# Performance work log

Measured on AMD Instinct MI355X. Metric: run time of the kernel, lower is better.

## Reference

```python
import jax, jax.numpy as jnp
import numpy as np

BATCH, SEQ, D = 128, 256, 64


def setup_inputs() -> dict:
    key = jax.random.key(0)
    k1, k2, k3 = jax.random.split(key, 3)
    eye = jnp.eye(D, dtype=jnp.float32)
    return {
        "x": jax.random.normal(k1, (BATCH, D), dtype=jnp.float32),
        "U_t": jax.random.normal(k2, (BATCH, SEQ, D), dtype=jnp.float32),
        "Y_t": jax.random.normal(k3, (BATCH, SEQ, D), dtype=jnp.float32),
        # learnable params, 'identity' init per module
        "F_mat": eye,
        "B_mat": eye,
        "H": eye,
        "LQ": jnp.tril(eye),
        "LR": jnp.tril(eye),
    }


def _kalman(x, U_t, Y_t, F_mat, B_mat, H, LQ, LR):
    d = x.shape[-1]
    bsz = x.shape[0]
    Q = LQ @ LQ.T                      # [D,D] process noise cov
    R = LR @ LR.T                      # [D,D] measurement noise cov
    I = jnp.eye(d, dtype=x.dtype)
    P0 = jnp.broadcast_to(I, (bsz, d, d))

    def step(carry, inp):
        x_prev, P = carry              # [B,D], [B,D,D]
        u, y = inp                     # [B,D], [B,D,D]
        x_pred = x_prev @ F_mat.T + u @ B_mat.T
        P_pred = F_mat @ P @ F_mat.T + Q            # broadcasts [D,D]@[B,D,D]
        S = H @ P_pred @ H.T + R                    # [B,D,D]
        S_inv = jnp.linalg.inv(S)
        K = P_pred @ (H.T @ S_inv)                  # Kalman gain [B,D,D]
        innov = y - x_pred @ H.T                    # [B,D]
        # matches torch: (innov.unsqueeze(1) @ K).squeeze(1)
        x_new = x_pred + jnp.einsum('bd,bde->be', innov, K)
        IKH = I - K @ H
        P_new = IKH @ P_pred @ jnp.swapaxes(IKH, -1, -2) \
              + K @ R @ jnp.swapaxes(K, -1, -2)
        P_new = 0.5 * (P_new + jnp.swapaxes(P_new, -1, -2))  # symmetrize
        return (x_new, P_new), (x_new, P_new)

    inputs = (jnp.swapaxes(U_t, 0, 1), jnp.swapaxes(Y_t, 0, 1))  # [S,B,D]
    _, (preds, covs) = jax.lax.scan(step, (x, P0), inputs)
    # prediction [B,S,D], covariance [B,S,D,D]
    return jnp.swapaxes(preds, 0, 1), jnp.swapaxes(covs, 0, 1)


def reference(x, U_t, Y_t, F_mat, B_mat, H, LQ, LR):
    return _kalman(x, U_t, Y_t, F_mat, B_mat, H, LQ, LR)
```

## Files before the change

kernel.cpp:

```cpp
#include <hip/hip_runtime.h>

#define BATCH 128
#define SEQ   256

#define WS_K  16
#define WS_A  (16 + SEQ * 4096)
#define WS_BP (WS_A + 4096)
#define WS_KS (WS_BP + 4096)

typedef unsigned short u16;
typedef float  f32x4v __attribute__((ext_vector_type(4)));
typedef __bf16 bf16x8 __attribute__((ext_vector_type(8)));
typedef unsigned short u16x8 __attribute__((ext_vector_type(8)));

struct Acc { f32x4v t[2][2]; };

__device__ __forceinline__ u16 bf16hi(float x) {
  unsigned u = __float_as_uint(x);
  return (u16)((u + 0x7fffu + ((u >> 16) & 1u)) >> 16);
}
__device__ __forceinline__ float bf16f(u16 h) {
  return __uint_as_float(((unsigned)h) << 16);
}

__device__ __forceinline__ int swadr(int a, int c) {
  return a * 64 + ((c ^ (a & 7)) << 3);
}

__device__ __forceinline__ bf16x8 frag(const u16* M, int strip, int kb, int q, int ln) {
  return *(const bf16x8*)(M + swadr(strip * 16 + ln, kb * 4 + q));
}

__device__ __forceinline__ void mm(const u16* As, const u16* Bs, Acc& acc,
                                   int R, int Cb, int q, int ln) {
#pragma unroll
  for (int kb = 0; kb < 2; ++kb) {
    bf16x8 ah[2], al[2], bh[2], bl[2];
#pragma unroll
    for (int i = 0; i < 2; ++i) {
      ah[i] = frag(As,        2 * R  + i, kb, q, ln);
      al[i] = frag(As + 4096, 2 * R  + i, kb, q, ln);
      bh[i] = frag(Bs,        2 * Cb + i, kb, q, ln);
      bl[i] = frag(Bs + 4096, 2 * Cb + i, kb, q, ln);
    }
#pragma unroll
    for (int i = 0; i < 2; ++i)
#pragma unroll
      for (int j = 0; j < 2; ++j) {
        acc.t[i][j] = __builtin_amdgcn_mfma_f32_16x16x32_bf16(ah[i], bh[j], acc.t[i][j], 0, 0, 0);
        acc.t[i][j] = __builtin_amdgcn_mfma_f32_16x16x32_bf16(ah[i], bl[j], acc.t[i][j], 0, 0, 0);
        acc.t[i][j] = __builtin_amdgcn_mfma_f32_16x16x32_bf16(al[i], bh[j], acc.t[i][j], 0, 0, 0);
      }
  }
}

__device__ __forceinline__ Acc accZero() {
  Acc a;
#pragma unroll
  for (int i = 0; i < 2; ++i)
#pragma unroll
    for (int j = 0; j < 2; ++j) {
      f32x4v z; z.x = 0.f; z.y = 0.f; z.z = 0.f; z.w = 0.f;
      a.t[i][j] = z;
    }
  return a;
}

__device__ __forceinline__ void storeC(float* dst, const Acc& a, int R, int Cb, int q, int ln) {
#pragma unroll
  for (int i = 0; i < 2; ++i)
#pragma unroll
    for (int j = 0; j < 2; ++j)
#pragma unroll
      for (int k = 0; k < 4; ++k)
        dst[(32 * R + 16 * i + 4 * q + k) * 64 + 32 * Cb + 16 * j + ln] = a.t[i][j][k];
}

__device__ __forceinline__ void emit16(const float* v, int row, int cb, u16* Rs, u16* Ts) {
  u16 h[16], lo[16];
#pragma unroll
  for (int e = 0; e < 16; ++e) {
    h[e] = bf16hi(v[e]);
    lo[e] = bf16hi(v[e] - bf16f(h[e]));
  }
  if (Rs) {
#pragma unroll
    for (int c = 0; c < 2; ++c) {
      u16x8 vh, vl;
#pragma unroll
      for (int e = 0; e < 8; ++e) { vh[e] = h[8 * c + e]; vl[e] = lo[8 * c + e]; }
      const int ad = swadr(row, (cb >> 3) + c);
      *(u16x8*)(Rs + ad) = vh;
      *(u16x8*)(Rs + 4096 + ad) = vl;
    }
  }
  if (Ts) {
    const int rc = row >> 3, rr = row & 7;
#pragma unroll
    for (int e = 0; e < 16; ++e) {
      const int a = cb + e;
      const int ad = a * 64 + ((rc ^ (a & 7)) << 3) + rr;
      Ts[ad] = h[e];
      Ts[4096 + ad] = lo[e];
    }
  }
}

__device__ __forceinline__ void splitsrc(const float* src, u16* Rs, u16* Ts,
                                         int mode, float scale, float dval, int tid) {
  const int row = tid >> 2, cb = (tid & 3) << 4;
  float v[16];
#pragma unroll
  for (int m = 0; m < 4; ++m) {
    f32x4v x = *(const f32x4v*)(src + row * 64 + cb + 4 * m);
    v[4 * m] = x.x; v[4 * m + 1] = x.y; v[4 * m + 2] = x.z; v[4 * m + 3] = x.w;
  }
  if (mode == 1) {
#pragma unroll
    for (int e = 0; e < 16; ++e) v[e] *= scale;
  } else if (mode == 2) {
#pragma unroll
    for (int e = 0; e < 16; ++e) v[e] = (((cb + e) == row) ? dval : 0.f) - v[e];
  }
  emit16(v, row, cb, Rs, Ts);
}

__device__ __forceinline__ float redmax(float v, float* red, int tid) {
#pragma unroll
  for (int off = 32; off > 0; off >>= 1) v = fmaxf(v, __shfl_xor(v, off));
  if ((tid & 63) == 0) red[300 + (tid >> 6)] = v;
  __syncthreads();
  float m = fmaxf(fmaxf(red[300], red[301]), fmaxf(red[302], red[303]));
  __syncthreads();
  return m;
}

__device__ __forceinline__ float dot4(float4 a, float4 b, float acc) {
  return fmaf(a.x, b.x, fmaf(a.y, b.y, fmaf(a.z, b.z, fmaf(a.w, b.w, acc))));
}

__global__ void __launch_bounds__(256, 1)
k1_riccati(const float* __restrict__ Fg, const float* __restrict__ Bg,
           const float* __restrict__ Hg, const float* __restrict__ LQg,
           const float* __restrict__ LRg, float* __restrict__ ws,
           float* __restrict__ covs) {
  __shared__ __align__(16) u16 smb[7 * 8192];
  __shared__ __align__(16) float Mf32[4096];
  __shared__ __align__(16) float Ppf32[4096];
  __shared__ __align__(16) float red[308];

  const int tid = threadIdx.x;
  const int l = tid & 63, w = tid >> 6, q = l >> 4, ln = l & 15;
  const int R = w >> 1, Cb = w & 1;

  {
    const int row = tid >> 2, cb = (tid & 3) << 4;
    float od = 0.f;
    const float* mats[5] = {Fg, Bg, Hg, LQg, LRg};
#pragma unroll
    for (int mi = 0; mi < 5; ++mi) {
      const float* M = mats[mi];
#pragma unroll
      for (int m = 0; m < 4; ++m) {
        f32x4v x = *(const f32x4v*)(M + row * 64 + cb + 4 * m);
        const int j0c = cb + 4 * m;
        if (j0c + 0 != row) od = fmaxf(od, fabsf(x.x));
        if (j0c + 1 != row) od = fmaxf(od, fabsf(x.y));
        if (j0c + 2 != row) od = fmaxf(od, fabsf(x.z));
        if (j0c + 3 != row) od = fmaxf(od, fabsf(x.w));
      }
    }
    const float odall = redmax(od, red, tid);
    if (odall == 0.f) {
      if (tid < 64) {
        const int e = tid;
        const float f = Fg[e * 65], b = Bg[e * 65], h = Hg[e * 65];
        const float lq = LQg[e * 65], lr = LRg[e * 65];
        const float qv = lq * lq, rv = lr * lr;
        float p = 1.f, kprev = 0.f, kcur = 0.f, om = 1.f;
        int tstar = SEQ - 1;
        for (int t = 0; t < SEQ; ++t) {
          const float pp = f * p * f + qv;
          const float s = h * pp * h + rv;
          const float k = pp * h / s;
          const float kh = k * h;
          const float omv = 1.f - kh;
          const float pn = omv * omv * pp + k * k * rv;
          float* Kt = ws + WS_K + (size_t)t * 4096 + e * 64;
          float* Ct = covs + (size_t)t * 4096 + e * 64;
          f32x4v z; z.x = 0.f; z.y = 0.f; z.z = 0.f; z.w = 0.f;
#pragma unroll
          for (int m = 0; m < 16; ++m) {
            *(f32x4v*)(Kt + 4 * m) = z;
            *(f32x4v*)(Ct + 4 * m) = z;
          }
          Kt[e] = k;
          Ct[e] = pn;
          float dk = (t == 0) ? 1e9f : fabsf(k - kprev);
#pragma unroll
          for (int off = 32; off > 0; off >>= 1) dk = fmaxf(dk, __shfl_xor(dk, off));
          p = pn; kprev = k; kcur = k; om = omv;
          if (dk < 1e-3f) { tstar = t; break; }
        }
        {
          const float astar = om * f, bpv = om * b;
          float* Ar = ws + WS_A + e * 64;
          float* Bp = ws + WS_BP + e * 64;
          float* Ks = ws + WS_KS + e * 64;
          f32x4v z; z.x = 0.f; z.y = 0.f; z.z = 0.f; z.w = 0.f;
#pragma unroll
          for (int m = 0; m < 16; ++m) {
            *(f32x4v*)(Ar + 4 * m) = z;
            *(f32x4v*)(Bp + 4 * m) = z;
            *(f32x4v*)(Ks + 4 * m) = z;
          }
          Ar[e] = astar; Bp[e] = bpv; Ks[e] = kcur;
          const float a2 = astar * astar, a4 = a2 * a2, a8 = a4 * a4;
          float a16 = fabsf(a8 * a8);
#pragma unroll
          for (int off = 32; off > 0; off >>= 1) a16 = fmaxf(a16, __shfl_xor(a16, off));
          if (e == 0) {
            ((int*)ws)[0] = tstar;
            ((int*)ws)[1] = (tstar <= 16 && a16 < 1e-5f) ? 1 : 0;
          }
        }
      }
      return;
    }
  }

  u16* SF = smb;
  u16* SH = smb + 8192;
  u16* SX = smb + 2 * 8192;
  u16* S1 = smb + 3 * 8192;
  u16* S2 = smb + 4 * 8192;
  u16* S3 = smb + 5 * 8192;
  u16* S4 = smb + 6 * 8192;

  splitsrc(Fg, SF, nullptr, 0, 0, 0, tid);
  splitsrc(Hg, SH, nullptr, 0, 0, 0, tid);
  splitsrc(LQg, S1, nullptr, 0, 0, 0, tid);
  __syncthreads();
  Acc qacc = accZero(); mm(S1, S1, qacc, R, Cb, q, ln);
  __syncthreads();
  splitsrc(LRg, S1, nullptr, 0, 0, 0, tid);
  __syncthreads();
  Acc racc = accZero(); mm(S1, S1, racc, R, Cb, q, ln);
  __syncthreads();
  {
    const int row = tid >> 2, cb = (tid & 3) << 4;
    float v[16];
#pragma unroll
    for (int e = 0; e < 16; ++e) v[e] = ((cb + e) == row) ? 1.f : 0.f;
    emit16(v, row, cb, S4, nullptr);
  }
  __syncthreads();

  int tstar = SEQ - 1;
  for (int t = 0; t < SEQ; ++t) {
    const u16* Wsrc = SF;
    if (t > 0) {
      Acc a = accZero(); mm(SF, S4, a, R, Cb, q, ln);
      storeC(Mf32, a, R, Cb, q, ln);
      __syncthreads();
      splitsrc(Mf32, S1, nullptr, 0, 0, 0, tid);
      __syncthreads();
      Wsrc = S1;
    }
    {
      Acc a = qacc; mm(Wsrc, SF, a, R, Cb, q, ln);
      storeC(Ppf32, a, R, Cb, q, ln);
      __syncthreads();
      splitsrc(Ppf32, S2, nullptr, 0, 0, 0, tid);
      __syncthreads();
    }
    {
      Acc a = accZero(); mm(SH, S2, a, R, Cb, q, ln);
      storeC(Mf32, a, R, Cb, q, ln);
      __syncthreads();
      splitsrc(Mf32, S3, S4, 0, 0, 0, tid);
      __syncthreads();
    }
    {
      Acc a = racc; mm(S3, SH, a, R, Cb, q, ln);
      storeC(Mf32, a, R, Cb, q, ln);
      __syncthreads();
      if (t == 0) {
        const int col = tid & 63, grp = tid >> 6;
        float s = 0.f;
        for (int r2 = grp * 16; r2 < grp * 16 + 16; ++r2) s += fabsf(Mf32[r2 * 64 + col]);
        red[tid] = s;
        __syncthreads();
        if (tid < 64) {
          float cs = red[tid] + red[64 + tid] + red[128 + tid] + red[192 + tid];
#pragma unroll
          for (int off = 32; off > 0; off >>= 1) cs = fmaxf(cs, __shfl_xor(cs, off));
          if (tid == 0) red[256] = 1.f / (cs * cs);
        }
        __syncthreads();
        const float sc = red[256];
        splitsrc(Mf32, SX, nullptr, 1, sc, 0, tid);
        __syncthreads();
      }
      splitsrc(Mf32, S2, nullptr, 0, 0, 0, tid);
      __syncthreads();
    }
    const int cap = (t == 0) ? 40 : 4;
    for (int it = 0; it < cap; ++it) {
      Acc e_ = accZero(); mm(S2, SX, e_, R, Cb, q, ln);
      float r = 0.f;
#pragma unroll
      for (int i = 0; i < 2; ++i)
#pragma unroll
        for (int j = 0; j < 2; ++j)
#pragma unroll
          for (int k = 0; k < 4; ++k) {
            const int gr = 32 * R + 16 * i + 4 * q + k;
            const int gc = 32 * Cb + 16 * j + ln;
            r = fmaxf(r, fabsf(e_.t[i][j][k] - ((gr == gc) ? 1.f : 0.f)));
          }
      const float rall = redmax(r, red, tid);
      if (rall < 5e-4f) break;
      storeC(Mf32, e_, R, Cb, q, ln);
      __syncthreads();
      splitsrc(Mf32, nullptr, S1, 2, 0, 2.0f, tid);
      __syncthreads();
      Acc x2 = accZero(); mm(SX, S1, x2, R, Cb, q, ln);
      storeC(Mf32, x2, R, Cb, q, ln);
      __syncthreads();
      splitsrc(Mf32, SX, nullptr, 0, 0, 0, tid);
      __syncthreads();
      if (rall * rall < 1e-4f) break;
    }
    __syncthreads();
    float dk;
    {
      Acc a = accZero(); mm(SX, S4, a, R, Cb, q, ln);
      storeC(Mf32, a, R, Cb, q, ln);
      __syncthreads();
      const int row = tid >> 2, cb = (tid & 3) << 4;
      float v[16]; float dmax = (t == 0) ? 1e9f : 0.f;
      float* wrow = ws + WS_K + (size_t)t * 4096 + row * 64 + cb;
#pragma unroll
      for (int m = 0; m < 4; ++m) {
        f32x4v x = *(const f32x4v*)(Mf32 + row * 64 + cb + 4 * m);
        v[4 * m] = x.x; v[4 * m + 1] = x.y; v[4 * m + 2] = x.z; v[4 * m + 3] = x.w;
        *(f32x4v*)(wrow + 4 * m) = x;
      }
      if (t > 0) {
        const float* prow = wrow - 4096;
#pragma unroll
        for (int m = 0; m < 4; ++m) {
          f32x4v p = *(const f32x4v*)(prow + 4 * m);
          dmax = fmaxf(dmax, fmaxf(fmaxf(fabsf(v[4 * m] - p.x), fabsf(v[4 * m + 1] - p.y)),
                                   fmaxf(fabsf(v[4 * m + 2] - p.z), fabsf(v[4 * m + 3] - p.w))));
        }
      }
      emit16(v, row, cb, nullptr, S1);
      dk = redmax(dmax, red, tid);
    }
    {
      Acc a = accZero(); mm(S1, S4, a, R, Cb, q, ln);
      storeC(Mf32, a, R, Cb, q, ln);
      __syncthreads();
      const int row = tid >> 2, cb = (tid & 3) << 4;
      float pv[16];
#pragma unroll
      for (int m = 0; m < 4; ++m) {
        f32x4v mij = *(const f32x4v*)(Mf32 + row * 64 + cb + 4 * m);
        f32x4v pp  = *(const f32x4v*)(Ppf32 + row * 64 + cb + 4 * m);
        pv[4 * m]     = pp.x - 0.5f * (mij.x + Mf32[(cb + 4 * m + 0) * 64 + row]);
        pv[4 * m + 1] = pp.y - 0.5f * (mij.y + Mf32[(cb + 4 * m + 1) * 64 + row]);
        pv[4 * m + 2] = pp.z - 0.5f * (mij.z + Mf32[(cb + 4 * m + 2) * 64 + row]);
        pv[4 * m + 3] = pp.w - 0.5f * (mij.w + Mf32[(cb + 4 * m + 3) * 64 + row]);
      }
      float* crow = covs + (size_t)t * 4096 + row * 64 + cb;
#pragma unroll
      for (int m = 0; m < 4; ++m) {
        f32x4v o; o.x = pv[4 * m]; o.y = pv[4 * m + 1]; o.z = pv[4 * m + 2]; o.w = pv[4 * m + 3];
        *(f32x4v*)(crow + 4 * m) = o;
      }
      emit16(pv, row, cb, S4, nullptr);
      __syncthreads();
    }
    if (dk < 1e-3f) { tstar = t; break; }
  }

  {
    Acc a = accZero(); mm(S1, SH, a, R, Cb, q, ln);
    storeC(Mf32, a, R, Cb, q, ln);
    __syncthreads();
    splitsrc(Mf32, S2, nullptr, 2, 0, 1.0f, tid);
    __syncthreads();
  }
  splitsrc(Fg, nullptr, S3, 0, 0, 0, tid);
  __syncthreads();
  {
    Acc a = accZero(); mm(S2, S3, a, R, Cb, q, ln);
    storeC(Mf32, a, R, Cb, q, ln);
#pragma unroll
    for (int i = 0; i < 2; ++i)
#pragma unroll
      for (int j = 0; j < 2; ++j)
#pragma unroll
        for (int k = 0; k < 4; ++k)
          ws[WS_A + (size_t)((32 * R + 16 * i + 4 * q + k) * 64 + 32 * Cb + 16 * j + ln)] = a.t[i][j][k];
    __syncthreads();
    splitsrc(Mf32, S1, S4, 0, 0, 0, tid);
    __syncthreads();
  }
  splitsrc(Bg, nullptr, S3, 0, 0, 0, tid);
  __syncthreads();
  {
    Acc a = accZero(); mm(S2, S3, a, R, Cb, q, ln);
#pragma unroll
    for (int i = 0; i < 2; ++i)
#pragma unroll
      for (int j = 0; j < 2; ++j)
#pragma unroll
        for (int k = 0; k < 4; ++k)
          ws[WS_BP + (size_t)((32 * R + 16 * i + 4 * q + k) * 64 + 32 * Cb + 16 * j + ln)] = a.t[i][j][k];
  }
  {
    const int row = tid >> 2, cb = (tid & 3) << 4;
    const float* srcr = ws + WS_K + (size_t)tstar * 4096 + row * 64 + cb;
    float* dstr = ws + WS_KS + row * 64 + cb;
#pragma unroll
    for (int m = 0; m < 4; ++m) *(f32x4v*)(dstr + 4 * m) = *(const f32x4v*)(srcr + 4 * m);
  }
  __syncthreads();
  {
    Acc a = accZero(); mm(S1, S4, a, R, Cb, q, ln);
    storeC(Mf32, a, R, Cb, q, ln); __syncthreads();
    splitsrc(Mf32, S2, S3, 0, 0, 0, tid); __syncthreads();
  }
  {
    Acc a = accZero(); mm(S2, S3, a, R, Cb, q, ln);
    storeC(Mf32, a, R, Cb, q, ln); __syncthreads();
    splitsrc(Mf32, S1, S4, 0, 0, 0, tid); __syncthreads();
  }
  {
    Acc a = accZero(); mm(S1, S4, a, R, Cb, q, ln);
    storeC(Mf32, a, R, Cb, q, ln); __syncthreads();
    splitsrc(Mf32, S2, S3, 0, 0, 0, tid); __syncthreads();
  }
  {
    Acc a = accZero(); mm(S2, S3, a, R, Cb, q, ln);
    float am = 0.f;
#pragma unroll
    for (int i = 0; i < 2; ++i)
#pragma unroll
      for (int j = 0; j < 2; ++j)
#pragma unroll
        for (int k = 0; k < 4; ++k) am = fmaxf(am, fabsf(a.t[i][j][k]));
    const float amax = redmax(am, red, tid);
    if (tid == 0) {
      ((int*)ws)[0] = tstar;
      ((int*)ws)[1] = (tstar <= 16 && amax < 1e-5f) ? 1 : 0;
    }
  }
}

#define NB2 512
#define NX2 1024

__global__ void __launch_bounds__(256, 4)
k2_fused(const float* __restrict__ x0, const float* __restrict__ U,
         const float* __restrict__ Y, const float* __restrict__ Fg,
         const float* __restrict__ Bg, const float* __restrict__ Hg,
         const float* __restrict__ ws, float* __restrict__ preds,
         float* __restrict__ covs) {
  const int tid = threadIdx.x;
  const int wg = blockIdx.x;
  const int tstar = ((const int*)ws)[0];
  const int flag  = ((const int*)ws)[1];

  if (wg < NB2) {
    const int s = wg >> 1, half = wg & 1;
    const int se = (s < tstar) ? s : tstar;
    const float4* src = (const float4*)(covs + (size_t)se * 4096);
    float4 r0 = src[tid], r1 = src[256 + tid], r2 = src[512 + tid], r3 = src[768 + tid];
    const int b0 = half << 6;
    for (int b = b0; b < b0 + 64; ++b) {
      if (b == 0 && s <= tstar) continue;
      float4* dst = (float4*)(covs + ((size_t)b * SEQ + s) * 4096);
      dst[tid] = r0; dst[256 + tid] = r1; dst[512 + tid] = r2; dst[768 + tid] = r3;
    }
  } else {
    const int xw = wg - NB2;
    const int c = xw >> 7, b = xw & 127;
    const int e = tid >> 2, q = tid & 3;
    const int co = q << 4;
    __shared__ __align__(16) float xv[64], xp[64], inn[64], us[2][64], ys[2][64];

    if (c == 0) {
      const int t1 = flag ? 32 : SEQ;
      float4 Fr[4], Br[4], Hr[4], Kr[4];
      {
        const float4* fp = (const float4*)(Fg + e * 64 + co);
        const float4* bp = (const float4*)(Bg + e * 64 + co);
        const float4* hp = (const float4*)(Hg + e * 64 + co);
#pragma unroll
        for (int m = 0; m < 4; ++m) { Fr[m] = fp[m]; Br[m] = bp[m]; Hr[m] = hp[m]; }
      }
      if (tid < 64) xv[tid] = x0[b * 64 + tid];
      int staged = -1;
      for (int t = 0; t < t1; ++t) {
        const int se = (t < tstar) ? t : tstar;
        if (se != staged) {
          const float4* kp = (const float4*)(ws + WS_K + (size_t)se * 4096 + e * 64 + co);
#pragma unroll
          for (int m = 0; m < 4; ++m) Kr[m] = kp[m];
          staged = se;
        }
        if (tid < 64) us[0][tid] = U[((size_t)b * SEQ + t) * 64 + tid];
        else if (tid < 128) ys[0][tid - 64] = Y[((size_t)b * SEQ + t) * 64 + (tid - 64)];
        __syncthreads();
        const float4* xv4 = (const float4*)xv;
        const float4* us4 = (const float4*)us[0];
        float v = 0.f;
#pragma unroll
        for (int m = 0; m < 4; ++m) {
          v = dot4(Fr[m], xv4[q * 4 + m], v);
          v = dot4(Br[m], us4[q * 4 + m], v);
        }
        v += __shfl_xor(v, 1); v += __shfl_xor(v, 2);
        if (q == 0) xp[e] = v;
        __syncthreads();
        const float4* xp4 = (const float4*)xp;
        float wv = 0.f;
#pragma unroll
        for (int m = 0; m < 4; ++m) wv = dot4(Hr[m], xp4[q * 4 + m], wv);
        wv += __shfl_xor(wv, 1); wv += __shfl_xor(wv, 2);
        if (q == 0) inn[e] = ys[0][e] - wv;
        __syncthreads();
        const float4* in4 = (const float4*)inn;
        float z = 0.f;
#pragma unroll
        for (int m = 0; m < 4; ++m) z = dot4(Kr[m], in4[q * 4 + m], z);
        z += __shfl_xor(z, 1); z += __shfl_xor(z, 2);
        if (q == 0) xv[e] = xp[e] + z;
        __syncthreads();
        if (tid < 64) preds[((size_t)b * SEQ + t) * 64 + tid] = xv[tid];
      }
    } else {
      if (!flag) return;
      const int tb = 32 * c - 16, out0 = 32 * c, t1 = 32 * c + 32;
      float4 Ar[4], Pr[4], Sr[4];
      {
        const float4* ap = (const float4*)(ws + WS_A + e * 64 + co);
        const float4* pp = (const float4*)(ws + WS_BP + e * 64 + co);
        const float4* sp = (const float4*)(ws + WS_KS + e * 64 + co);
#pragma unroll
        for (int m = 0; m < 4; ++m) { Ar[m] = ap[m]; Pr[m] = pp[m]; Sr[m] = sp[m]; }
      }
      if (tid < 64) xv[tid] = 0.f;
      float g = 0.f;
      if (tid < 64) g = U[((size_t)b * SEQ + tb) * 64 + tid];
      else if (tid < 128) g = Y[((size_t)b * SEQ + tb) * 64 + (tid - 64)];
      int pb = 0;
      for (int t = tb; t < t1; ++t) {
        if (tid < 64) us[pb][tid] = g;
        else if (tid < 128) ys[pb][tid - 64] = g;
        __syncthreads();
        if (t + 1 < t1) {
          if (tid < 64) g = U[((size_t)b * SEQ + (t + 1)) * 64 + tid];
          else if (tid < 128) g = Y[((size_t)b * SEQ + (t + 1)) * 64 + (tid - 64)];
        }
        const float4* xv4 = (const float4*)xv;
        const float4* us4 = (const float4*)us[pb];
        const float4* ys4 = (const float4*)ys[pb];
        float v = 0.f;
#pragma unroll
        for (int m = 0; m < 4; ++m) {
          v = dot4(Ar[m], xv4[q * 4 + m], v);
          v = dot4(Pr[m], us4[q * 4 + m], v);
          v = dot4(Sr[m], ys4[q * 4 + m], v);
        }
        v += __shfl_xor(v, 1); v += __shfl_xor(v, 2);
        if (t >= out0 && q == 0) preds[((size_t)b * SEQ + t) * 64 + e] = v;
        __syncthreads();
        if (q == 0) xv[e] = v;
        pb ^= 1;
      }
    }
  }
}

extern "C" void kernel_launch(void* const* d_in, const int* in_sizes, int n_in,
                              void* d_out, int out_size, void* d_ws, size_t ws_size,
                              hipStream_t stream) {
  (void)in_sizes; (void)n_in; (void)out_size; (void)ws_size;
  const float* x0 = (const float*)d_in[0];
  const float* U  = (const float*)d_in[1];
  const float* Y  = (const float*)d_in[2];
  const float* F  = (const float*)d_in[3];
  const float* B  = (const float*)d_in[4];
  const float* H  = (const float*)d_in[5];
  const float* LQ = (const float*)d_in[6];
  const float* LR = (const float*)d_in[7];
  float* preds = (float*)d_out;
  float* covs  = preds + (size_t)BATCH * SEQ * 64;
  float* ws    = (float*)d_ws;

  hipLaunchKernelGGL(k1_riccati, dim3(1), dim3(256), 0, stream,
                     F, B, H, LQ, LR, ws, covs);
  hipLaunchKernelGGL(k2_fused, dim3(NB2 + NX2), dim3(256), 0, stream,
                     x0, U, Y, F, B, H, ws, preds, covs);
}
```

Before: 599.7 us.

## Reassign covariance broadcast per batch and ping-pong state to halve barriers

The covariance-broadcast workgroups are remapped so that each one owns a batch and a quarter of the sequence instead of a sequence step and half the batches. Steps after the steady-state index reuse register-held data, and earlier steps copy from the source. The chunked state-propagation loop now double-buffers the state vector and stages the next step's inputs before the single barrier, which cuts barriers per step from two to one. The new mapping gives contiguous writes per workgroup but adds per-step global reads for steps before steady state.

```diff
diff --git a/kernel.cpp b/kernel.cpp
--- a/kernel.cpp
+++ b/kernel.cpp
@@ -476,22 +476,28 @@
   const int flag  = ((const int*)ws)[1];
 
   if (wg < NB2) {
-    const int s = wg >> 1, half = wg & 1;
-    const int se = (s < tstar) ? s : tstar;
-    const float4* src = (const float4*)(covs + (size_t)se * 4096);
-    float4 r0 = src[tid], r1 = src[256 + tid], r2 = src[512 + tid], r3 = src[768 + tid];
-    const int b0 = half << 6;
-    for (int b = b0; b < b0 + 64; ++b) {
-      if (b == 0 && s <= tstar) continue;
+    const int b = wg >> 2, qt = wg & 3;
+    const int s0 = qt << 6;
+    const float4* srcInf = (const float4*)(covs + (size_t)tstar * 4096);
+    float4 r0 = srcInf[tid], r1 = srcInf[256 + tid];
+    float4 r2 = srcInf[512 + tid], r3 = srcInf[768 + tid];
+    for (int s = s0; s < s0 + 64; ++s) {
       float4* dst = (float4*)(covs + ((size_t)b * SEQ + s) * 4096);
-      dst[tid] = r0; dst[256 + tid] = r1; dst[512 + tid] = r2; dst[768 + tid] = r3;
+      if (s <= tstar) {
+        if (b == 0) continue;
+        const float4* src = (const float4*)(covs + (size_t)s * 4096);
+        dst[tid] = src[tid]; dst[256 + tid] = src[256 + tid];
+        dst[512 + tid] = src[512 + tid]; dst[768 + tid] = src[768 + tid];
+      } else {
+        dst[tid] = r0; dst[256 + tid] = r1; dst[512 + tid] = r2; dst[768 + tid] = r3;
+      }
     }
   } else {
     const int xw = wg - NB2;
     const int c = xw >> 7, b = xw & 127;
     const int e = tid >> 2, q = tid & 3;
     const int co = q << 4;
-    __shared__ __align__(16) float xv[64], xp[64], inn[64], us[2][64], ys[2][64];
+    __shared__ __align__(16) float xa[64], xb[64], inn[64], us[2][64], ys[2][64];
 
     if (c == 0) {
       const int t1 = flag ? 32 : SEQ;
@@ -503,7 +509,7 @@
 #pragma unroll
         for (int m = 0; m < 4; ++m) { Fr[m] = fp[m]; Br[m] = bp[m]; Hr[m] = hp[m]; }
       }
-      if (tid < 64) xv[tid] = x0[b * 64 + tid];
+      if (tid < 64) xa[tid] = x0[b * 64 + tid];
       int staged = -1;
       for (int t = 0; t < t1; ++t) {
         const int se = (t < tstar) ? t : tstar;
@@ -516,7 +522,7 @@
         if (tid < 64) us[0][tid] = U[((size_t)b * SEQ + t) * 64 + tid];
         else if (tid < 128) ys[0][tid - 64] = Y[((size_t)b * SEQ + t) * 64 + (tid - 64)];
         __syncthreads();
-        const float4* xv4 = (const float4*)xv;
+        const float4* xv4 = (const float4*)xa;
         const float4* us4 = (const float4*)us[0];
         float v = 0.f;
 #pragma unroll
@@ -525,9 +531,9 @@
           v = dot4(Br[m], us4[q * 4 + m], v);
         }
         v += __shfl_xor(v, 1); v += __shfl_xor(v, 2);
-        if (q == 0) xp[e] = v;
-        __syncthreads();
-        const float4* xp4 = (const float4*)xp;
+        if (q == 0) xb[e] = v;
+        __syncthreads();
+        const float4* xp4 = (const float4*)xb;
         float wv = 0.f;
 #pragma unroll
         for (int m = 0; m < 4; ++m) wv = dot4(Hr[m], xp4[q * 4 + m], wv);
@@ -539,9 +545,9 @@
 #pragma unroll
         for (int m = 0; m < 4; ++m) z = dot4(Kr[m], in4[q * 4 + m], z);
         z += __shfl_xor(z, 1); z += __shfl_xor(z, 2);
-        if (q == 0) xv[e] = xp[e] + z;
-        __syncthreads();
-        if (tid < 64) preds[((size_t)b * SEQ + t) * 64 + tid] = xv[tid];
+        if (q == 0) xa[e] = xb[e] + z;
+        __syncthreads();
+        if (tid < 64) preds[((size_t)b * SEQ + t) * 64 + tid] = xa[tid];
       }
     } else {
       if (!flag) return;
@@ -554,20 +560,22 @@
 #pragma unroll
         for (int m = 0; m < 4; ++m) { Ar[m] = ap[m]; Pr[m] = pp[m]; Sr[m] = sp[m]; }
       }
-      if (tid < 64) xv[tid] = 0.f;
+      float* xcur = xa;
+      float* xnxt = xb;
+      if (tid < 64) xcur[tid] = 0.f;
       float g = 0.f;
       if (tid < 64) g = U[((size_t)b * SEQ + tb) * 64 + tid];
       else if (tid < 128) g = Y[((size_t)b * SEQ + tb) * 64 + (tid - 64)];
+      if (tid < 64) us[0][tid] = g;
+      else if (tid < 128) ys[0][tid - 64] = g;
+      if (tb + 1 < t1) {
+        if (tid < 64) g = U[((size_t)b * SEQ + tb + 1) * 64 + tid];
+        else if (tid < 128) g = Y[((size_t)b * SEQ + tb + 1) * 64 + (tid - 64)];
+      }
+      __syncthreads();
       int pb = 0;
       for (int t = tb; t < t1; ++t) {
-        if (tid < 64) us[pb][tid] = g;
-        else if (tid < 128) ys[pb][tid - 64] = g;
-        __syncthreads();
-        if (t + 1 < t1) {
-          if (tid < 64) g = U[((size_t)b * SEQ + (t + 1)) * 64 + tid];
-          else if (tid < 128) g = Y[((size_t)b * SEQ + (t + 1)) * 64 + (tid - 64)];
-        }
-        const float4* xv4 = (const float4*)xv;
+        const float4* xv4 = (const float4*)xcur;
         const float4* us4 = (const float4*)us[pb];
         const float4* ys4 = (const float4*)ys[pb];
         float v = 0.f;
@@ -578,9 +586,18 @@
           v = dot4(Sr[m], ys4[q * 4 + m], v);
         }
         v += __shfl_xor(v, 1); v += __shfl_xor(v, 2);
+        if (q == 0) xnxt[e] = v;
         if (t >= out0 && q == 0) preds[((size_t)b * SEQ + t) * 64 + e] = v;
-        __syncthreads();
-        if (q == 0) xv[e] = v;
+        if (t + 1 < t1) {
+          if (tid < 64) us[pb ^ 1][tid] = g;
+          else if (tid < 128) ys[pb ^ 1][tid - 64] = g;
+          if (t + 2 < t1) {
+            if (tid < 64) g = U[((size_t)b * SEQ + t + 2) * 64 + tid];
+            else if (tid < 128) g = Y[((size_t)b * SEQ + t + 2) * 64 + (tid - 64)];
+          }
+        }
+        __syncthreads();
+        { float* tp = xcur; xcur = xnxt; xnxt = tp; }
         pb ^= 1;
       }
     }
```

New measurement: 604.2 us. Within noise of the previous version (+0.7%).
